# Kernel optimization log

Hardware: AMD Instinct MI355X
Metric: run time of the kernel (lower is better)

Reference implementation:

```python
import jax, jax.numpy as jnp
import numpy as np

NUM_PITCHES = 88
H_FEAT = 188
LSTM_UNITS = 48
N_STATES = 5
CTX_HID = 16
CTX_OUT = 4


def _glorot(key, shape):
    fan_in, fan_out = shape[1], shape[0]
    lim = (6.0 / (fan_in + fan_out)) ** 0.5
    return jax.random.uniform(key, shape, jnp.float32, -lim, lim)


def setup_inputs() -> dict:
    key = jax.random.key(0)
    ks = jax.random.split(key, 16)
    B, T = 16, 256
    pitch_features = jax.random.normal(ks[0], (B, NUM_PITCHES, H_FEAT, T), jnp.float32)
    prev_context = jax.random.uniform(ks[1], (B, NUM_PITCHES, 3), jnp.float32)
    # context net params
    fc1_w = _glorot(ks[2], (CTX_HID, 3)); fc1_b = jnp.zeros((CTX_HID,), jnp.float32)
    fc2_w = _glorot(ks[3], (CTX_HID, CTX_HID)); fc2_b = jnp.zeros((CTX_HID,), jnp.float32)
    fc3_w = _glorot(ks[4], (CTX_OUT, CTX_HID)); fc3_b = jnp.zeros((CTX_OUT,), jnp.float32)
    # lstm1: input H_FEAT+4 -> 48; gates order i,f,g,o (torch convention)
    in1 = H_FEAT + CTX_OUT
    lstm1_wih = _glorot(ks[5], (4 * LSTM_UNITS, in1))
    lstm1_whh = _glorot(ks[6], (4 * LSTM_UNITS, LSTM_UNITS))
    lstm1_bih = jnp.zeros((4 * LSTM_UNITS,), jnp.float32)
    lstm1_bhh = jnp.zeros((4 * LSTM_UNITS,), jnp.float32)
    lstm2_wih = _glorot(ks[7], (4 * LSTM_UNITS, LSTM_UNITS))
    lstm2_whh = _glorot(ks[8], (4 * LSTM_UNITS, LSTM_UNITS))
    lstm2_bih = jnp.zeros((4 * LSTM_UNITS,), jnp.float32)
    lstm2_bhh = jnp.zeros((4 * LSTM_UNITS,), jnp.float32)
    fc_states_w = _glorot(ks[9], (N_STATES, LSTM_UNITS))
    fc_states_b = jnp.zeros((N_STATES,), jnp.float32)
    return dict(pitch_features=pitch_features, prev_context=prev_context,
                fc1_w=fc1_w, fc1_b=fc1_b, fc2_w=fc2_w, fc2_b=fc2_b,
                fc3_w=fc3_w, fc3_b=fc3_b,
                lstm1_wih=lstm1_wih, lstm1_whh=lstm1_whh, lstm1_bih=lstm1_bih, lstm1_bhh=lstm1_bhh,
                lstm2_wih=lstm2_wih, lstm2_whh=lstm2_whh, lstm2_bih=lstm2_bih, lstm2_bhh=lstm2_bhh,
                fc_states_w=fc_states_w, fc_states_b=fc_states_b)


def _lstm_scan(x, wih, whh, bih, bhh):
    # x: (S, N, In); zero init state; returns (S, N, U)
    S, N, _ = x.shape
    U = whh.shape[1]
    xg = jnp.einsum('sni,gi->sng', x, wih) + bih + bhh  # precompute input gates

    def step(carry, xg_t):
        h, c = carry
        g = xg_t + h @ whh.T  # (N, 4U)
        i, f, gg, o = jnp.split(g, 4, axis=-1)
        c = jax.nn.sigmoid(f) * c + jax.nn.sigmoid(i) * jnp.tanh(gg)
        h = jax.nn.sigmoid(o) * jnp.tanh(c)
        return (h, c), h

    init = (jnp.zeros((N, U), x.dtype), jnp.zeros((N, U), x.dtype))
    _, hs = jax.lax.scan(step, init, xg)
    return hs


def reference(pitch_features, prev_context,
              fc1_w, fc1_b, fc2_w, fc2_b, fc3_w, fc3_b,
              lstm1_wih, lstm1_whh, lstm1_bih, lstm1_bhh,
              lstm2_wih, lstm2_whh, lstm2_bih, lstm2_bhh,
              fc_states_w, fc_states_b):
    B, P, H, T = pitch_features.shape
    # Context net (context never updates across t in the original loop)
    x = jax.nn.relu(prev_context @ fc1_w.T + fc1_b)
    x = jax.nn.relu(x @ fc2_w.T + fc2_b)
    ctx_emb = x @ fc3_w.T + fc3_b  # (B, P, 4)
    # Each timestep t is independent: LSTM runs over the pitch axis (len 88)
    # with zero initial state every step. Fold (B, T) into batch N.
    pf = jnp.transpose(pitch_features, (1, 0, 3, 2)).reshape(P, B * T, H)  # (P, BT, H)
    ce = jnp.broadcast_to(ctx_emb[:, None, :, :], (B, T, P, CTX_OUT))
    ce = jnp.transpose(ce, (2, 0, 1, 3)).reshape(P, B * T, CTX_OUT)
    seq = jnp.concatenate([pf, ce], axis=-1)  # (P, BT, H+4)
    h = _lstm_scan(seq, lstm1_wih, lstm1_whh, lstm1_bih, lstm1_bhh)
    h = _lstm_scan(h, lstm2_wih, lstm2_whh, lstm2_bih, lstm2_bhh)
    logits = h @ fc_states_w.T + fc_states_b  # (P, BT, 5)
    logits = logits.reshape(P, B, T, N_STATES)
    logits = jnp.transpose(logits, (1, 0, 3, 2))  # (B, P, 5, T)
    return jax.nn.softmax(logits, axis=2)
```

## Files before the change

### kernel.cpp

```cpp
#include <hip/hip_runtime.h>
#include <hip/hip_bf16.h>
#include <cstdint>

#define P_ 88
#define B_ 16
#define T_ 256
#define H_ 188
#define G_ 192
#define U_ 48
#define N_ 4096

typedef __attribute__((ext_vector_type(8))) _Float16 f16x8;
typedef __attribute__((ext_vector_type(4))) float f32x4;

__device__ __forceinline__ float sigf(float x) {
  return __builtin_amdgcn_rcpf(1.0f + __expf(-x));
}
__device__ __forceinline__ float tanh_f(float x) {
  return 1.0f - 2.0f * __builtin_amdgcn_rcpf(1.0f + __expf(2.0f * x));
}

__device__ __forceinline__ void lds_barrier() {
  asm volatile("s_waitcnt lgkmcnt(0)\n\ts_barrier" ::: "memory");
}

__global__ void ctx_kernel(const float* __restrict__ pc,
                           const float* __restrict__ fc1w, const float* __restrict__ fc1b,
                           const float* __restrict__ fc2w, const float* __restrict__ fc2b,
                           const float* __restrict__ fc3w, const float* __restrict__ fc3b,
                           const float* __restrict__ wih1,
                           const float* __restrict__ bih1, const float* __restrict__ bhh1,
                           float* __restrict__ ctxg) {
  int bp = blockIdx.x * 64 + threadIdx.x;
  if (bp >= B_ * P_) return;
  float p0 = pc[bp * 3 + 0], p1 = pc[bp * 3 + 1], p2 = pc[bp * 3 + 2];
  float x1[16], x2[16];
#pragma unroll
  for (int jj = 0; jj < 16; ++jj)
    x1[jj] = fmaxf(0.f, fc1w[jj * 3 + 0] * p0 + fc1w[jj * 3 + 1] * p1 + fc1w[jj * 3 + 2] * p2 + fc1b[jj]);
#pragma unroll
  for (int jj = 0; jj < 16; ++jj) {
    float s = fc2b[jj];
#pragma unroll
    for (int i = 0; i < 16; ++i) s += fc2w[jj * 16 + i] * x1[i];
    x2[jj] = fmaxf(0.f, s);
  }
  float ce[4];
#pragma unroll
  for (int jj = 0; jj < 4; ++jj) {
    float s = fc3b[jj];
#pragma unroll
    for (int i = 0; i < 16; ++i) s += fc3w[jj * 16 + i] * x2[i];
    ce[jj] = s;
  }
  float* op = ctxg + (size_t)bp * G_;
  for (int g = 0; g < G_; ++g) {
    const float* wr = wih1 + (size_t)g * G_ + H_;
    op[g] = bih1[g] + bhh1[g] + ce[0] * wr[0] + ce[1] * wr[1] + ce[2] * wr[2] + ce[3] * wr[3];
  }
}

__global__ __launch_bounds__(256, 2) void scan_fused(
    const float* __restrict__ pf, const float* __restrict__ ctxg,
    const float* __restrict__ wih1, const float* __restrict__ whh1,
    const float* __restrict__ wih2, const float* __restrict__ whh2,
    const float* __restrict__ bih2, const float* __restrict__ bhh2,
    const float* __restrict__ fcw, const float* __restrict__ fcb,
    float* __restrict__ out) {
  __shared__ __align__(16) _Float16 h12[16][104];
  __shared__ __align__(16) float gs1[8][196];
  __shared__ __align__(16) float gs2[8][196];
  __shared__ __align__(16) float h2f[8][52];
  __shared__ __align__(16) float fcws[5 * 48];
  __shared__ float logit_s[5][8];
  __shared__ float prob_s[5][8];
  __shared__ __align__(16) _Float16 pfhi[2][8][200];
  __shared__ __align__(16) _Float16 pflo[2][8][200];

  const int tid = threadIdx.x;
  const int w = tid >> 6, l = tid & 63;
  const int lj = l & 15, lq = l >> 4;
  const int g512 = (blockIdx.x & 7) * 64 + (blockIdx.x >> 3);
  const int n0 = g512 * 8;
  const int b = n0 >> 8, t0 = n0 & 255;

  f16x8 b1[3][2];
  f16x8 b2f[3][3];
  f16x8 wf[3][6];
  float bias2r[3];
#pragma unroll
  for (int i = 0; i < 3; ++i) {
    const int j = w * 48 + i * 16 + lj;
    bias2r[i] = bih2[j] + bhh2[j];
#pragma unroll
    for (int kc = 0; kc < 2; ++kc)
#pragma unroll
      for (int e = 0; e < 8; ++e) {
        const int u = kc * 32 + lq * 8 + e;
        b1[i][kc][e] = (u < U_) ? (_Float16)whh1[j * U_ + u] : (_Float16)0.f;
      }
#pragma unroll
    for (int kc = 0; kc < 3; ++kc)
#pragma unroll
      for (int e = 0; e < 8; ++e) {
        const int k = kc * 32 + lq * 8 + e;
        b2f[i][kc][e] = (k < U_) ? (_Float16)wih2[j * U_ + k]
                                 : (_Float16)whh2[j * U_ + (k - U_)];
      }
#pragma unroll
    for (int kc = 0; kc < 6; ++kc)
#pragma unroll
      for (int e = 0; e < 8; ++e) {
        const int k = kc * 32 + lq * 8 + e;
        wf[i][kc][e] = (k < H_) ? (_Float16)wih1[(size_t)j * G_ + k] : (_Float16)0.f;
      }
  }

  for (int e = tid; e < 16 * 104 / 2; e += 256) ((unsigned*)h12)[e] = 0u;
  for (int e = tid; e < 1600; e += 256) {
    ((unsigned*)pfhi)[e] = 0u;
    ((unsigned*)pflo)[e] = 0u;
  }
  for (int e = tid; e < 5 * U_; e += 256) fcws[e] = fcw[e];
  lds_barrier();

  const int tn0 = tid / U_, tu0 = tid % U_;
  const int tn1 = (256 + tid) / U_, tu1 = (256 + tid) % U_;
  const bool has2 = (tid < 128);
  float c1s[2] = {0.f, 0.f}, c2s[2] = {0.f, 0.f};

  const bool fcth = tid < 40;
  const int fk = tid >> 3, fn = tid & 7;
  const float fcbr = fcth ? fcb[fk] : 0.f;
  const bool stth = tid >= 96 && tid < 136;
  const int sk = (tid - 96) >> 3, sn = (tid - 96) & 7;
  const bool smth = tid >= 192 && tid < 200;
  const int smn = tid - 192;

  const int sh = tid >> 3, stl = tid & 7;
  const float* pfb = pf + (size_t)b * P_ * H_ * T_ + (size_t)sh * T_ + t0 + stl;

#pragma unroll
  for (int it = 0; it < 6; ++it) {
    const int h = sh + it * 32;
    if (h < H_) {
      const float v0 = pfb[(size_t)it * 32 * T_];
      const float v1 = pfb[(size_t)H_ * T_ + (size_t)it * 32 * T_];
      const _Float16 h0 = (_Float16)v0, h1 = (_Float16)v1;
      pfhi[0][stl][h] = h0; pflo[0][stl][h] = (_Float16)(v0 - (float)h0);
      pfhi[1][stl][h] = h1; pflo[1][stl][h] = (_Float16)(v1 - (float)h1);
    }
  }
  lds_barrier();

  const float* cgbase = ctxg + (size_t)b * P_ * G_ + w * 48 + lj;
  float cgN[3];
  f32x4 xgC[3];
#pragma unroll
  for (int i = 0; i < 3; ++i) {
    const float c0 = cgbase[i * 16];
    xgC[i][0] = c0; xgC[i][1] = c0; xgC[i][2] = c0; xgC[i][3] = c0;
    cgN[i] = cgbase[G_ + i * 16];
  }
  const float* cgp = cgbase + 2 * G_;

#define INGEMM(ACC, RB)                                                        \
  {                                                                            \
    _Pragma("unroll") for (int c = 0; c < 6; ++c) {                            \
      const f16x8 ah = *(const f16x8*)&pfhi[RB][lj & 7][c * 32 + lq * 8];      \
      const f16x8 al = *(const f16x8*)&pflo[RB][lj & 7][c * 32 + lq * 8];      \
      ACC[0] = __builtin_amdgcn_mfma_f32_16x16x32_f16(ah, wf[0][c], ACC[0], 0, 0, 0); \
      ACC[1] = __builtin_amdgcn_mfma_f32_16x16x32_f16(ah, wf[1][c], ACC[1], 0, 0, 0); \
      ACC[2] = __builtin_amdgcn_mfma_f32_16x16x32_f16(ah, wf[2][c], ACC[2], 0, 0, 0); \
      ACC[0] = __builtin_amdgcn_mfma_f32_16x16x32_f16(al, wf[0][c], ACC[0], 0, 0, 0); \
      ACC[1] = __builtin_amdgcn_mfma_f32_16x16x32_f16(al, wf[1][c], ACC[1], 0, 0, 0); \
      ACC[2] = __builtin_amdgcn_mfma_f32_16x16x32_f16(al, wf[2][c], ACC[2], 0, 0, 0); \
    }                                                                          \
  }

  INGEMM(xgC, 0);
  lds_barrier();

  const float* pfstage = pfb + (size_t)2 * H_ * T_;

  for (int p = -1; p < P_; ++p) {
    const bool doL2 = (p >= 0), doL1 = (p < P_ - 1);
    const bool doProd = (p <= 85), doStage = (p <= 84);
    const int prb = p & 1;
    const int pwb = prb ^ 1;

    float pv[6];
    if (doStage) {
#pragma unroll
      for (int it = 0; it < 6; ++it)
        pv[it] = (sh + it * 32 < H_) ? pfstage[(size_t)it * 32 * T_] : 0.f;
    }

    const _Float16* hr = &h12[lj][0];
    const f16x8 f0 = *(const f16x8*)(hr + lq * 8);
    const f16x8 f1 = *(const f16x8*)(hr + 32 + lq * 8);
    if (doL2) {
      const f16x8 f2 = *(const f16x8*)(hr + 64 + lq * 8);
      f32x4 dH[3];
#pragma unroll
      for (int i = 0; i < 3; ++i) {
        dH[i][0] = bias2r[i]; dH[i][1] = bias2r[i];
        dH[i][2] = bias2r[i]; dH[i][3] = bias2r[i];
      }
#pragma unroll
      for (int i = 0; i < 3; ++i)
        dH[i] = __builtin_amdgcn_mfma_f32_16x16x32_f16(f0, b2f[i][0], dH[i], 0, 0, 0);
#pragma unroll
      for (int i = 0; i < 3; ++i)
        dH[i] = __builtin_amdgcn_mfma_f32_16x16x32_f16(f1, b2f[i][1], dH[i], 0, 0, 0);
#pragma unroll
      for (int i = 0; i < 3; ++i)
        dH[i] = __builtin_amdgcn_mfma_f32_16x16x32_f16(f2, b2f[i][2], dH[i], 0, 0, 0);
      if (lq < 2) {
#pragma unroll
        for (int i = 0; i < 3; ++i)
#pragma unroll
          for (int r = 0; r < 4; ++r)
            gs2[lq * 4 + r][w * 48 + i * 16 + lj] = dH[i][r];
      }
    }
    if (fcth && p >= 1) {
      float a = fcbr;
#pragma unroll
      for (int uq = 0; uq < 12; ++uq) {
        f32x4 hv = *(const f32x4*)&h2f[fn][uq * 4];
        f32x4 wv = *(const f32x4*)&fcws[fk * 48 + uq * 4];
        a += hv[0] * wv[0] + hv[1] * wv[1] + hv[2] * wv[2] + hv[3] * wv[3];
      }
      logit_s[fk][fn] = a;
    }
    if (stth && p >= 2) {
      out[(((size_t)b * P_ + (p - 2)) * 5 + sk) * T_ + t0 + sn] = prob_s[sk][sn];
    }
    __builtin_amdgcn_sched_barrier(0);
    if (doL1) {
      f32x4 cH[3];
#pragma unroll
      for (int i = 0; i < 3; ++i)
        cH[i] = __builtin_amdgcn_mfma_f32_16x16x32_f16(f0, b1[i][0], xgC[i], 0, 0, 0);
#pragma unroll
      for (int i = 0; i < 3; ++i)
        cH[i] = __builtin_amdgcn_mfma_f32_16x16x32_f16(f1, b1[i][1], cH[i], 0, 0, 0);
      if (lq < 2) {
#pragma unroll
        for (int i = 0; i < 3; ++i)
#pragma unroll
          for (int r = 0; r < 4; ++r)
            gs1[lq * 4 + r][w * 48 + i * 16 + lj] = cH[i][r];
      }
    }
    if (doProd) {
      f32x4 xgP[3];
#pragma unroll
      for (int i = 0; i < 3; ++i) {
        xgP[i][0] = cgN[i]; xgP[i][1] = cgN[i];
        xgP[i][2] = cgN[i]; xgP[i][3] = cgN[i];
      }
      INGEMM(xgP, prb);
      if (doStage) {
#pragma unroll
        for (int i = 0; i < 3; ++i) cgN[i] = cgp[i * 16];
        cgp += G_;
      }
#pragma unroll
      for (int i = 0; i < 3; ++i) xgC[i] = xgP[i];
    }
    if (doStage) {
#pragma unroll
      for (int it = 0; it < 6; ++it) {
        const int h = sh + it * 32;
        if (h < H_) {
          const _Float16 hi = (_Float16)pv[it];
          pfhi[pwb][stl][h] = hi;
          pflo[pwb][stl][h] = (_Float16)(pv[it] - (float)hi);
        }
      }
      pfstage += (size_t)H_ * T_;
    }
    lds_barrier();
    if (doL2) {
      {
        const int n = tn0, u = tu0;
        const float ig = gs2[n][u], fg = gs2[n][48 + u];
        const float gg = gs2[n][96 + u], og = gs2[n][144 + u];
        const float cc = sigf(fg) * c2s[0] + sigf(ig) * tanh_f(gg);
        c2s[0] = cc;
        const float h = sigf(og) * tanh_f(cc);
        h12[n][48 + u] = (_Float16)h;
        h2f[n][u] = h;
      }
      if (has2) {
        const int n = tn1, u = tu1;
        const float ig = gs2[n][u], fg = gs2[n][48 + u];
        const float gg = gs2[n][96 + u], og = gs2[n][144 + u];
        const float cc = sigf(fg) * c2s[1] + sigf(ig) * tanh_f(gg);
        c2s[1] = cc;
        const float h = sigf(og) * tanh_f(cc);
        h12[n][48 + u] = (_Float16)h;
        h2f[n][u] = h;
      }
    }
    if (doL1) {
      {
        const int n = tn0, u = tu0;
        const float ig = gs1[n][u], fg = gs1[n][48 + u];
        const float gg = gs1[n][96 + u], og = gs1[n][144 + u];
        const float cc = sigf(fg) * c1s[0] + sigf(ig) * tanh_f(gg);
        c1s[0] = cc;
        h12[n][u] = (_Float16)(sigf(og) * tanh_f(cc));
      }
      if (has2) {
        const int n = tn1, u = tu1;
        const float ig = gs1[n][u], fg = gs1[n][48 + u];
        const float gg = gs1[n][96 + u], og = gs1[n][144 + u];
        const float cc = sigf(fg) * c1s[1] + sigf(ig) * tanh_f(gg);
        c1s[1] = cc;
        h12[n][u] = (_Float16)(sigf(og) * tanh_f(cc));
      }
    }
    if (smth && p >= 1) {
      const int n = smn;
      const float l0 = logit_s[0][n], l1 = logit_s[1][n], l2 = logit_s[2][n],
                  l3 = logit_s[3][n], l4 = logit_s[4][n];
      const float m = fmaxf(fmaxf(fmaxf(l0, l1), fmaxf(l2, l3)), l4);
      const float e0 = __expf(l0 - m), e1 = __expf(l1 - m), e2 = __expf(l2 - m),
                  e3 = __expf(l3 - m), e4 = __expf(l4 - m);
      const float rs = __builtin_amdgcn_rcpf(e0 + e1 + e2 + e3 + e4);
      prob_s[0][n] = e0 * rs; prob_s[1][n] = e1 * rs; prob_s[2][n] = e2 * rs;
      prob_s[3][n] = e3 * rs; prob_s[4][n] = e4 * rs;
    }
    lds_barrier();
  }
  if (fcth) {
    float a = fcbr;
#pragma unroll
    for (int uq = 0; uq < 12; ++uq) {
      f32x4 hv = *(const f32x4*)&h2f[fn][uq * 4];
      f32x4 wv = *(const f32x4*)&fcws[fk * 48 + uq * 4];
      a += hv[0] * wv[0] + hv[1] * wv[1] + hv[2] * wv[2] + hv[3] * wv[3];
    }
    logit_s[fk][fn] = a;
  }
  if (stth) {
    out[(((size_t)b * P_ + (P_ - 2)) * 5 + sk) * T_ + t0 + sn] = prob_s[sk][sn];
  }
  lds_barrier();
  if (smth) {
    const int n = smn;
    const float l0 = logit_s[0][n], l1 = logit_s[1][n], l2 = logit_s[2][n],
                l3 = logit_s[3][n], l4 = logit_s[4][n];
    const float m = fmaxf(fmaxf(fmaxf(l0, l1), fmaxf(l2, l3)), l4);
    const float e0 = __expf(l0 - m), e1 = __expf(l1 - m), e2 = __expf(l2 - m),
                e3 = __expf(l3 - m), e4 = __expf(l4 - m);
    const float rs = __builtin_amdgcn_rcpf(e0 + e1 + e2 + e3 + e4);
    prob_s[0][n] = e0 * rs; prob_s[1][n] = e1 * rs; prob_s[2][n] = e2 * rs;
    prob_s[3][n] = e3 * rs; prob_s[4][n] = e4 * rs;
  }
  lds_barrier();
  if (stth) {
    out[(((size_t)b * P_ + (P_ - 1)) * 5 + sk) * T_ + t0 + sn] = prob_s[sk][sn];
  }
}

extern "C" void kernel_launch(void* const* d_in, const int* in_sizes, int n_in,
                              void* d_out, int out_size, void* d_ws, size_t ws_size,
                              hipStream_t stream) {
  const float* pf   = (const float*)d_in[0];
  const float* pc   = (const float*)d_in[1];
  const float* fc1w = (const float*)d_in[2];
  const float* fc1b = (const float*)d_in[3];
  const float* fc2w = (const float*)d_in[4];
  const float* fc2b = (const float*)d_in[5];
  const float* fc3w = (const float*)d_in[6];
  const float* fc3b = (const float*)d_in[7];
  const float* wih1 = (const float*)d_in[8];
  const float* whh1 = (const float*)d_in[9];
  const float* bih1 = (const float*)d_in[10];
  const float* bhh1 = (const float*)d_in[11];
  const float* wih2 = (const float*)d_in[12];
  const float* whh2 = (const float*)d_in[13];
  const float* bih2 = (const float*)d_in[14];
  const float* bhh2 = (const float*)d_in[15];
  const float* fcw  = (const float*)d_in[16];
  const float* fcb  = (const float*)d_in[17];
  float* out = (float*)d_out;

  float* ctxg = (float*)d_ws;

  ctx_kernel<<<22, 64, 0, stream>>>(pc, fc1w, fc1b, fc2w, fc2b, fc3w, fc3b,
                                    wih1, bih1, bhh1, ctxg);
  scan_fused<<<N_ / 8, 256, 0, stream>>>(pf, ctxg, wih1, whh1, wih2, whh2,
                                         bih2, bhh2, fcw, fcb, out);
}
```

Measured before the change: 392.3 us.

## Compute input-gate GEMM for two pitch steps per MFMA using all 16 rows

The input projection MFMA previously used only 8 of its 16 A-rows, duplicating the 8 timesteps. Now two consecutive pitch steps are packed into the 16 rows, so the input GEMM runs every other step. The two halves are split between lanes with shuffles, and the staging buffers are enlarged to hold four pitch slices. This halves the input-projection MFMA work, at the cost of more LDS, extra shuffles and more complex buffer indexing.

```diff
diff --git a/kernel.cpp b/kernel.cpp
--- a/kernel.cpp
+++ b/kernel.cpp
@@ -74,8 +74,8 @@
   __shared__ __align__(16) float fcws[5 * 48];
   __shared__ float logit_s[5][8];
   __shared__ float prob_s[5][8];
-  __shared__ __align__(16) _Float16 pfhi[2][8][200];
-  __shared__ __align__(16) _Float16 pflo[2][8][200];
+  __shared__ __align__(16) _Float16 pfhi[2][16][200];
+  __shared__ __align__(16) _Float16 pflo[2][16][200];
 
   const int tid = threadIdx.x;
   const int w = tid >> 6, l = tid & 63;
@@ -117,7 +117,7 @@
   }
 
   for (int e = tid; e < 16 * 104 / 2; e += 256) ((unsigned*)h12)[e] = 0u;
-  for (int e = tid; e < 1600; e += 256) {
+  for (int e = tid; e < 3200; e += 256) {
     ((unsigned*)pfhi)[e] = 0u;
     ((unsigned*)pflo)[e] = 0u;
   }
@@ -141,34 +141,33 @@
   const float* pfb = pf + (size_t)b * P_ * H_ * T_ + (size_t)sh * T_ + t0 + stl;
 
 #pragma unroll
-  for (int it = 0; it < 6; ++it) {
-    const int h = sh + it * 32;
-    if (h < H_) {
-      const float v0 = pfb[(size_t)it * 32 * T_];
-      const float v1 = pfb[(size_t)H_ * T_ + (size_t)it * 32 * T_];
-      const _Float16 h0 = (_Float16)v0, h1 = (_Float16)v1;
-      pfhi[0][stl][h] = h0; pflo[0][stl][h] = (_Float16)(v0 - (float)h0);
-      pfhi[1][stl][h] = h1; pflo[1][stl][h] = (_Float16)(v1 - (float)h1);
+  for (int s = 0; s < 4; ++s) {
+    const int bufi = (s >> 1) & 1, row = (s & 1) * 8 + stl;
+    const float* sp = pfb + (size_t)s * H_ * T_;
+#pragma unroll
+    for (int it = 0; it < 6; ++it) {
+      const int h = sh + it * 32;
+      if (h < H_) {
+        const float v = sp[(size_t)it * 32 * T_];
+        const _Float16 hi = (_Float16)v;
+        pfhi[bufi][row][h] = hi;
+        pflo[bufi][row][h] = (_Float16)(v - (float)hi);
+      }
     }
   }
   lds_barrier();
 
   const float* cgbase = ctxg + (size_t)b * P_ * G_ + w * 48 + lj;
-  float cgN[3];
-  f32x4 xgC[3];
-#pragma unroll
-  for (int i = 0; i < 3; ++i) {
-    const float c0 = cgbase[i * 16];
-    xgC[i][0] = c0; xgC[i][1] = c0; xgC[i][2] = c0; xgC[i][3] = c0;
-    cgN[i] = cgbase[G_ + i * 16];
-  }
-  const float* cgp = cgbase + 2 * G_;
-
-#define INGEMM(ACC, RB)                                                        \
+
+#define INGEMM(ACC, RB, CE, CO)                                                \
   {                                                                            \
+    _Pragma("unroll") for (int i = 0; i < 3; ++i) {                            \
+      const float bsel = (l < 32) ? (CE)[i] : (CO)[i];                         \
+      ACC[i][0] = bsel; ACC[i][1] = bsel; ACC[i][2] = bsel; ACC[i][3] = bsel;  \
+    }                                                                          \
     _Pragma("unroll") for (int c = 0; c < 6; ++c) {                            \
-      const f16x8 ah = *(const f16x8*)&pfhi[RB][lj & 7][c * 32 + lq * 8];      \
-      const f16x8 al = *(const f16x8*)&pflo[RB][lj & 7][c * 32 + lq * 8];      \
+      const f16x8 ah = *(const f16x8*)&pfhi[RB][lj][c * 32 + lq * 8];          \
+      const f16x8 al = *(const f16x8*)&pflo[RB][lj][c * 32 + lq * 8];          \
       ACC[0] = __builtin_amdgcn_mfma_f32_16x16x32_f16(ah, wf[0][c], ACC[0], 0, 0, 0); \
       ACC[1] = __builtin_amdgcn_mfma_f32_16x16x32_f16(ah, wf[1][c], ACC[1], 0, 0, 0); \
       ACC[2] = __builtin_amdgcn_mfma_f32_16x16x32_f16(ah, wf[2][c], ACC[2], 0, 0, 0); \
@@ -178,16 +177,31 @@
     }                                                                          \
   }
 
-  INGEMM(xgC, 0);
+  f32x4 xgA[3], xgB[3];
+  {
+    float cgE[3], cgO[3];
+#pragma unroll
+    for (int i = 0; i < 3; ++i) { cgE[i] = cgbase[i * 16]; cgO[i] = cgbase[G_ + i * 16]; }
+    f32x4 xgP[3];
+    INGEMM(xgP, 0, cgE, cgO);
+#pragma unroll
+    for (int i = 0; i < 3; ++i) {
+      xgA[i] = xgP[i];
+#pragma unroll
+      for (int r = 0; r < 4; ++r) xgB[i][r] = __shfl_xor((float)xgP[i][r], 32);
+    }
+  }
   lds_barrier();
 
-  const float* pfstage = pfb + (size_t)2 * H_ * T_;
+  const float* cgp = cgbase + 2 * G_;
+  const float* pfstage = pfb + (size_t)4 * H_ * T_;
 
   for (int p = -1; p < P_; ++p) {
     const bool doL2 = (p >= 0), doL1 = (p < P_ - 1);
-    const bool doProd = (p <= 85), doStage = (p <= 84);
-    const int prb = p & 1;
-    const int pwb = prb ^ 1;
+    const bool doProd = ((p & 1) == 0) && (p <= 84);
+    const bool doStage = (p >= 0 && p <= 83);
+    const int prodRB = ((p + 2) >> 1) & 1;
+    const int stgRB = ((p + 4) >> 1) & 1, stgRow = ((p + 4) & 1) * 8 + stl;
 
     float pv[6];
     if (doStage) {
@@ -241,8 +255,10 @@
     if (doL1) {
       f32x4 cH[3];
 #pragma unroll
-      for (int i = 0; i < 3; ++i)
-        cH[i] = __builtin_amdgcn_mfma_f32_16x16x32_f16(f0, b1[i][0], xgC[i], 0, 0, 0);
+      for (int i = 0; i < 3; ++i) {
+        const f32x4 xc = (p & 1) ? xgA[i] : xgB[i];
+        cH[i] = __builtin_amdgcn_mfma_f32_16x16x32_f16(f0, b1[i][0], xc, 0, 0, 0);
+      }
 #pragma unroll
       for (int i = 0; i < 3; ++i)
         cH[i] = __builtin_amdgcn_mfma_f32_16x16x32_f16(f1, b1[i][1], cH[i], 0, 0, 0);
@@ -255,20 +271,18 @@
       }
     }
     if (doProd) {
+      float cgE[3], cgO[3];
+#pragma unroll
+      for (int i = 0; i < 3; ++i) { cgE[i] = cgp[i * 16]; cgO[i] = cgp[G_ + i * 16]; }
+      cgp += 2 * G_;
       f32x4 xgP[3];
+      INGEMM(xgP, prodRB, cgE, cgO);
 #pragma unroll
       for (int i = 0; i < 3; ++i) {
-        xgP[i][0] = cgN[i]; xgP[i][1] = cgN[i];
-        xgP[i][2] = cgN[i]; xgP[i][3] = cgN[i];
-      }
-      INGEMM(xgP, prb);
-      if (doStage) {
-#pragma unroll
-        for (int i = 0; i < 3; ++i) cgN[i] = cgp[i * 16];
-        cgp += G_;
-      }
-#pragma unroll
-      for (int i = 0; i < 3; ++i) xgC[i] = xgP[i];
+        xgA[i] = xgP[i];
+#pragma unroll
+        for (int r = 0; r < 4; ++r) xgB[i][r] = __shfl_xor((float)xgP[i][r], 32);
+      }
     }
     if (doStage) {
 #pragma unroll
@@ -276,8 +290,8 @@
         const int h = sh + it * 32;
         if (h < H_) {
           const _Float16 hi = (_Float16)pv[it];
-          pfhi[pwb][stl][h] = hi;
-          pflo[pwb][stl][h] = (_Float16)(pv[it] - (float)hi);
+          pfhi[stgRB][stgRow][h] = hi;
+          pflo[stgRB][stgRow][h] = (_Float16)(pv[it] - (float)hi);
         }
       }
       pfstage += (size_t)H_ * T_;
```

Result: faster. 367.0 us (-6.5%).
